# Kernel tuning notes

Measured on AMD Instinct MI355X. Metric: run time of the kernel, lower is better.

## Reference

```python
import jax, jax.numpy as jnp
import numpy as np

B, N, D, H = 8, 1024, 1024, 16
DH = D // H
SCALE = DH ** -0.5
NEG = -1e9


def setup_inputs() -> dict:
    key = jax.random.key(0)
    k1, k2, k3, k4 = jax.random.split(key, 4)
    x = jax.random.normal(k1, (B, N, D), dtype=jnp.float32)
    mask = jax.random.randint(k2, (B, N), 0, 2, dtype=jnp.int32)
    w_qkv = jax.random.normal(k3, (D, 3 * D), dtype=jnp.float32) * (D ** -0.5)
    w_out = jax.random.normal(k4, (D, D), dtype=jnp.float32) * (D ** -0.5)
    b_out = jnp.zeros((D,), dtype=jnp.float32)
    return {"x": x, "mask": mask, "w_qkv": w_qkv, "w_out": w_out, "b_out": b_out}


def reference(x, mask, w_qkv, w_out, b_out):
    b, n, d = x.shape
    qkv = x @ w_qkv  # [b, n, 3d]
    q, k, v = jnp.split(qkv, 3, axis=-1)
    # [b, n, d] -> [b, h, n, dh]
    reshape = lambda t: t.reshape(b, n, H, DH).transpose(0, 2, 1, 3)
    q, k, v = reshape(q), reshape(k), reshape(v)
    dots = jnp.einsum("bhqd,bhkd->bhqk", q, k) * SCALE  # [b, h, n, n]
    # mask [b, n] -> [b, 1, n]; broadcasts over heads and query dim (masks keys)
    m = (mask == 0)[:, None, None, :]
    dots = jnp.where(m, NEG, dots)
    attn = jax.nn.softmax(dots, axis=-1)
    out = jnp.einsum("bhqk,bhkd->bhqd", attn, v)  # [b, h, n, dh]
    out = out.transpose(0, 2, 1, 3).reshape(b, n, d)  # [b, n, d]
    out = out @ w_out + b_out
    return out, attn
```

## Files before the change

kernel.cpp:

```cpp
#include <hip/hip_runtime.h>
#include <hip/hip_bf16.h>

typedef unsigned short u16;
typedef __attribute__((ext_vector_type(8))) short bf16x8;
typedef __attribute__((ext_vector_type(4))) float f32x4;

#define DEVI __device__ __forceinline__

constexpr float SCALE = 0.125f;

DEVI float bf2f(u16 u) { unsigned v = ((unsigned)u) << 16; float f; __builtin_memcpy(&f, &v, 4); return f; }
DEVI u16 f2bf(float f) { __hip_bfloat16 h = __float2bfloat16(f); u16 u; __builtin_memcpy(&u, &h, 2); return u; }

DEVI void gload_lds16(const u16* g, u16* l) {
    __builtin_amdgcn_global_load_lds(
        (const __attribute__((address_space(1))) unsigned int*)g,
        (__attribute__((address_space(3))) unsigned int*)l, 16, 0, 0);
}

__global__ __launch_bounds__(256) void cast_f32_bf16(const float* __restrict__ in,
                                                     u16* __restrict__ out, int n) {
    int i = (blockIdx.x * 256 + threadIdx.x) * 4;
    if (i >= n) return;
    float4 v = *(const float4*)(in + i);
    ushort4 o;
    o.x = f2bf(v.x); o.y = f2bf(v.y); o.z = f2bf(v.z); o.w = f2bf(v.w);
    *(ushort4*)(out + i) = o;
}

__global__ __launch_bounds__(256) void transpose_f32_bf16(const float* __restrict__ in,
                                                          u16* __restrict__ out,
                                                          int R, int C) {
    __shared__ u16 t[64][65];
    int r0 = blockIdx.y * 64, c0 = blockIdx.x * 64;
    int tid = threadIdx.x;
    for (int i = 0; i < 16; i++) {
        int idx = tid + i * 256; int r = idx >> 6, c = idx & 63;
        t[r][c] = f2bf(in[(size_t)(r0 + r) * C + c0 + c]);
    }
    __syncthreads();
    for (int i = 0; i < 16; i++) {
        int idx = tid + i * 256; int c = idx >> 6, r = idx & 63;
        out[(size_t)(c0 + c) * R + r0 + r] = t[r][c];
    }
}

__global__ __launch_bounds__(256) void make_vt(const u16* __restrict__ qkv,
                                               u16* __restrict__ vt) {
    __shared__ u16 t[64][65];
    int bh = blockIdx.y; int b = bh >> 4, h = bh & 15;
    int n0 = blockIdx.x * 64;
    int tid = threadIdx.x;
    const u16* src = qkv + (size_t)b * 1024 * 3072 + 2048 + h * 64;
    for (int i = 0; i < 16; i++) {
        int idx = tid + i * 256; int n = idx >> 6, d = idx & 63;
        t[n][d] = src[(size_t)(n0 + n) * 3072 + d];
    }
    __syncthreads();
    u16* dst = vt + (size_t)bh * 64 * 1024;
    for (int i = 0; i < 16; i++) {
        int idx = tid + i * 256; int d = idx >> 6, n = idx & 63;
        dst[(size_t)d * 1024 + n0 + n] = t[n][d];
    }
}

template <bool BIAS, bool F32OUT>
__global__ __launch_bounds__(256) void gemm_bt(const u16* __restrict__ A,
                                               const u16* __restrict__ Bt,
                                               const float* __restrict__ bias,
                                               void* __restrict__ Cv,
                                               int M, int N, int K) {
    __shared__ alignas(16) u16 As[128 * 64];
    __shared__ alignas(16) u16 Bs[128 * 64];
    int tid = threadIdx.x;
    int wave = tid >> 6, lane = tid & 63, quad = lane >> 4, lm = lane & 15;
    int bm = blockIdx.y * 128, bn = blockIdx.x * 128;
    int wm = (wave >> 1) * 64, wn = (wave & 1) * 64;

    f32x4 acc[4][4];
    for (int i = 0; i < 4; i++) for (int j = 0; j < 4; j++) acc[i][j] = f32x4{0.f, 0.f, 0.f, 0.f};

    int lrow8 = lane >> 3;
    int lcol  = (lane & 7) * 8;

    for (int kb = 0; kb < K; kb += 64) {
        for (int i = 0; i < 4; i++) {
            int c = wave * 4 + i;
            int row = c * 8 + lrow8;
            gload_lds16(A  + (size_t)(bm + row) * K + kb + lcol, &As[c * 512 + lane * 8]);
            gload_lds16(Bt + (size_t)(bn + row) * K + kb + lcol, &Bs[c * 512 + lane * 8]);
        }
        __syncthreads();
        for (int ks = 0; ks < 2; ks++) {
            bf16x8 af[4], bfr[4];
            for (int mt = 0; mt < 4; mt++)
                af[mt] = *(const bf16x8*)(&As[(wm + mt * 16 + lm) * 64 + ks * 32 + quad * 8]);
            for (int nt = 0; nt < 4; nt++)
                bfr[nt] = *(const bf16x8*)(&Bs[(wn + nt * 16 + lm) * 64 + ks * 32 + quad * 8]);
            for (int mt = 0; mt < 4; mt++)
                for (int nt = 0; nt < 4; nt++)
                    acc[mt][nt] = __builtin_amdgcn_mfma_f32_16x16x32_bf16(
                        af[mt], bfr[nt], acc[mt][nt], 0, 0, 0);
        }
        __syncthreads();
    }
    for (int mt = 0; mt < 4; mt++)
        for (int nt = 0; nt < 4; nt++) {
            int col = bn + wn + nt * 16 + lm;
            float bv = BIAS ? bias[col] : 0.f;
            for (int r = 0; r < 4; r++) {
                int row = bm + wm + mt * 16 + quad * 4 + r;
                if (F32OUT) ((float*)Cv)[(size_t)row * N + col] = acc[mt][nt][r] + bv;
                else        ((u16*)Cv)[(size_t)row * N + col] = f2bf(acc[mt][nt][r] + bv);
            }
        }
}

__global__ __launch_bounds__(256) void attn_mfma(const u16* __restrict__ qkv,
                                                 const u16* __restrict__ vt,
                                                 const int* __restrict__ mask,
                                                 float* __restrict__ attn_out,
                                                 u16* __restrict__ o_ws) {
    __shared__ alignas(16) u16 Ks[2 * 64 * 64];
    __shared__ alignas(16) u16 Vs[2 * 64 * 64];
    constexpr int LDP = 72;
    __shared__ alignas(16) u16 Ps[64 * LDP];

    int tid = threadIdx.x;
    int wave = tid >> 6, lane = tid & 63, quad = lane >> 4, lm = lane & 15;

    int flat = blockIdx.y * gridDim.x + blockIdx.x;
    int swz = (flat & 7) * 256 + (flat >> 3);
    int bh = swz >> 4, qb = swz & 15;
    int b = bh >> 4, h = bh & 15;
    int qrow0 = qb * 64 + wave * 16;

    int srow = lane >> 3;
    int scol = (((lane & 7) ^ srow) << 3);

    const u16* kbase  = qkv + (size_t)b * 1024 * 3072 + 1024 + h * 64;
    const u16* vtbase = vt + (size_t)bh * 64 * 1024;
    const int* mrow   = mask + b * 1024;

    for (int i = 0; i < 2; i++) {
        int c = wave * 2 + i;
        gload_lds16(kbase + (size_t)(c * 8 + srow) * 3072 + scol, &Ks[c * 512 + lane * 8]);
    }

    bf16x8 qf[2];
    {
        const u16* qptr = qkv + (size_t)(b * 1024 + qrow0 + lm) * 3072 + h * 64 + quad * 8;
        qf[0] = *(const bf16x8*)(qptr);
        qf[1] = *(const bf16x8*)(qptr + 32);
    }

    int fsw0 = ((0 * 4 + quad) ^ (lm & 7)) << 3;
    int fsw1 = ((1 * 4 + quad) ^ (lm & 7)) << 3;

    float l_r[4] = {0.f, 0.f, 0.f, 0.f};
    int cur = 0;
    for (int kb = 0; kb < 16; kb++) {
        __syncthreads();
        if (kb < 15) {
            int nb = (cur ^ 1) * 4096;
            for (int i = 0; i < 2; i++) {
                int c = wave * 2 + i;
                gload_lds16(kbase + (size_t)((kb + 1) * 64 + c * 8 + srow) * 3072 + scol,
                            &Ks[nb + c * 512 + lane * 8]);
            }
        }
        const u16* K0 = &Ks[cur * 4096];
        f32x4 acc[4];
        for (int nt = 0; nt < 4; nt++) acc[nt] = f32x4{0.f, 0.f, 0.f, 0.f};
        for (int nt = 0; nt < 4; nt++) {
            bf16x8 kf0 = *(const bf16x8*)(&K0[(nt * 16 + lm) * 64 + fsw0]);
            bf16x8 kf1 = *(const bf16x8*)(&K0[(nt * 16 + lm) * 64 + fsw1]);
            acc[nt] = __builtin_amdgcn_mfma_f32_16x16x32_bf16(qf[0], kf0, acc[nt], 0, 0, 0);
            acc[nt] = __builtin_amdgcn_mfma_f32_16x16x32_bf16(qf[1], kf1, acc[nt], 0, 0, 0);
        }
        for (int nt = 0; nt < 4; nt++) {
            bool mk = (mrow[kb * 64 + nt * 16 + lm] != 0);
            for (int r = 0; r < 4; r++)
                l_r[r] += mk ? __expf(acc[nt][r] * SCALE) : 0.f;
        }
        cur ^= 1;
    }
    float invl[4];
    for (int r = 0; r < 4; r++) {
        float l = l_r[r];
        for (int s = 8; s >= 1; s >>= 1) l += __shfl_xor(l, s, 64);
        invl[r] = 1.0f / l;
    }

    for (int i = 0; i < 2; i++) {
        int c = wave * 2 + i;
        gload_lds16(kbase + (size_t)(c * 8 + srow) * 3072 + scol, &Ks[c * 512 + lane * 8]);
        gload_lds16(vtbase + (size_t)(c * 8 + srow) * 1024 + scol, &Vs[c * 512 + lane * 8]);
    }

    f32x4 oacc[4];
    for (int nt = 0; nt < 4; nt++) oacc[nt] = f32x4{0.f, 0.f, 0.f, 0.f};
    cur = 0;
    for (int kb = 0; kb < 16; kb++) {
        __syncthreads();
        if (kb < 15) {
            int nb = (cur ^ 1) * 4096;
            for (int i = 0; i < 2; i++) {
                int c = wave * 2 + i;
                gload_lds16(kbase + (size_t)((kb + 1) * 64 + c * 8 + srow) * 3072 + scol,
                            &Ks[nb + c * 512 + lane * 8]);
                gload_lds16(vtbase + (size_t)(c * 8 + srow) * 1024 + (kb + 1) * 64 + scol,
                            &Vs[nb + c * 512 + lane * 8]);
            }
        }
        const u16* K0 = &Ks[cur * 4096];
        const u16* V0 = &Vs[cur * 4096];
        f32x4 acc[4];
        for (int nt = 0; nt < 4; nt++) acc[nt] = f32x4{0.f, 0.f, 0.f, 0.f};
        for (int nt = 0; nt < 4; nt++) {
            bf16x8 kf0 = *(const bf16x8*)(&K0[(nt * 16 + lm) * 64 + fsw0]);
            bf16x8 kf1 = *(const bf16x8*)(&K0[(nt * 16 + lm) * 64 + fsw1]);
            acc[nt] = __builtin_amdgcn_mfma_f32_16x16x32_bf16(qf[0], kf0, acc[nt], 0, 0, 0);
            acc[nt] = __builtin_amdgcn_mfma_f32_16x16x32_bf16(qf[1], kf1, acc[nt], 0, 0, 0);
        }
        for (int nt = 0; nt < 4; nt++) {
            bool mk = (mrow[kb * 64 + nt * 16 + lm] != 0);
            for (int r = 0; r < 4; r++) {
                float p = mk ? __expf(acc[nt][r] * SCALE) * invl[r] : 0.f;
                attn_out[((size_t)bh * 1024 + qb * 64 + wave * 16 + quad * 4 + r) * 1024
                         + kb * 64 + nt * 16 + lm] = p;
                Ps[(wave * 16 + quad * 4 + r) * LDP + nt * 16 + lm] = f2bf(p);
            }
        }
        for (int ks = 0; ks < 2; ks++) {
            bf16x8 pf = *(const bf16x8*)(&Ps[(wave * 16 + lm) * LDP + ks * 32 + quad * 8]);
            int fsw = (ks == 0) ? fsw0 : fsw1;
            for (int nt = 0; nt < 4; nt++) {
                bf16x8 vf = *(const bf16x8*)(&V0[(nt * 16 + lm) * 64 + fsw]);
                oacc[nt] = __builtin_amdgcn_mfma_f32_16x16x32_bf16(pf, vf, oacc[nt], 0, 0, 0);
            }
        }
        cur ^= 1;
    }
    for (int nt = 0; nt < 4; nt++)
        for (int r = 0; r < 4; r++) {
            int row = qb * 64 + wave * 16 + quad * 4 + r;
            o_ws[(size_t)(b * 1024 + row) * 1024 + h * 64 + nt * 16 + lm] = f2bf(oacc[nt][r]);
        }
}

extern "C" void kernel_launch(void* const* d_in, const int* in_sizes, int n_in,
                              void* d_out, int out_size, void* d_ws, size_t ws_size,
                              hipStream_t stream) {
    const float* x    = (const float*)d_in[0];
    const int*   mask = (const int*)d_in[1];
    const float* wqkv = (const float*)d_in[2];
    const float* wout = (const float*)d_in[3];
    const float* bout = (const float*)d_in[4];

    float* out  = (float*)d_out;
    float* attn = out + (size_t)8192 * 1024;

    char* ws = (char*)d_ws;
    u16* xbf   = (u16*)(ws);
    u16* vt    = xbf;
    u16* qkv   = (u16*)(ws + 16777216);
    u16* o_ws  = (u16*)(ws + 67108864);
    u16* wqkvT = (u16*)(ws + 83886080);
    u16* woutT = (u16*)(ws + 90177536);

    cast_f32_bf16<<<dim3(8192), 256, 0, stream>>>(x, xbf, 8388608);
    transpose_f32_bf16<<<dim3(48, 16), 256, 0, stream>>>(wqkv, wqkvT, 1024, 3072);
    transpose_f32_bf16<<<dim3(16, 16), 256, 0, stream>>>(wout, woutT, 1024, 1024);
    gemm_bt<false, false><<<dim3(24, 64), 256, 0, stream>>>(xbf, wqkvT, nullptr, qkv, 8192, 3072, 1024);
    make_vt<<<dim3(16, 128), 256, 0, stream>>>(qkv, vt);
    attn_mfma<<<dim3(16, 128), 256, 0, stream>>>(qkv, vt, mask, attn, o_ws);
    gemm_bt<true, true><<<dim3(8, 64), 256, 0, stream>>>(o_ws, woutT, bout, out, 8192, 1024, 1024);
}
```

Before: 836.9 us.

## Split attention into row-sum and PV kernels, XOR-swizzle P tile

Splits the two-pass attention kernel into two launches. The first computes softmax row sums and writes inverse denominators to workspace, reusing the wqkvT region after the QKV GEMM has consumed it. The second recomputes the scores, writes attention probabilities and accumulates P·V. The lighter first kernel needs less LDS and fewer registers, which should raise occupancy, and the padded P tile is replaced with an XOR-swizzled unpadded layout to avoid LDS bank conflicts. The cost is an extra launch and a small workspace round trip.

```diff
diff --git a/kernel.cpp b/kernel.cpp
--- a/kernel.cpp
+++ b/kernel.cpp
@@ -116,15 +116,10 @@
         }
 }
 
-__global__ __launch_bounds__(256) void attn_mfma(const u16* __restrict__ qkv,
-                                                 const u16* __restrict__ vt,
+__global__ __launch_bounds__(256) void attn_lsum(const u16* __restrict__ qkv,
                                                  const int* __restrict__ mask,
-                                                 float* __restrict__ attn_out,
-                                                 u16* __restrict__ o_ws) {
+                                                 float* __restrict__ invl_ws) {
     __shared__ alignas(16) u16 Ks[2 * 64 * 64];
-    __shared__ alignas(16) u16 Vs[2 * 64 * 64];
-    constexpr int LDP = 72;
-    __shared__ alignas(16) u16 Ps[64 * LDP];
 
     int tid = threadIdx.x;
     int wave = tid >> 6, lane = tid & 63, quad = lane >> 4, lm = lane & 15;
@@ -138,9 +133,8 @@
     int srow = lane >> 3;
     int scol = (((lane & 7) ^ srow) << 3);
 
-    const u16* kbase  = qkv + (size_t)b * 1024 * 3072 + 1024 + h * 64;
-    const u16* vtbase = vt + (size_t)bh * 64 * 1024;
-    const int* mrow   = mask + b * 1024;
+    const u16* kbase = qkv + (size_t)b * 1024 * 3072 + 1024 + h * 64;
+    const int* mrow  = mask + b * 1024;
 
     for (int i = 0; i < 2; i++) {
         int c = wave * 2 + i;
@@ -153,7 +147,6 @@
         qf[0] = *(const bf16x8*)(qptr);
         qf[1] = *(const bf16x8*)(qptr + 32);
     }
-
     int fsw0 = ((0 * 4 + quad) ^ (lm & 7)) << 3;
     int fsw1 = ((1 * 4 + quad) ^ (lm & 7)) << 3;
 
@@ -185,12 +178,39 @@
         }
         cur ^= 1;
     }
-    float invl[4];
-    for (int r = 0; r < 4; r++) {
-        float l = l_r[r];
-        for (int s = 8; s >= 1; s >>= 1) l += __shfl_xor(l, s, 64);
-        invl[r] = 1.0f / l;
-    }
+    for (int r = 0; r < 4; r++)
+        for (int s = 8; s >= 1; s >>= 1) l_r[r] += __shfl_xor(l_r[r], s, 64);
+    if (lm == 0) {
+        float4 v; v.x = 1.f / l_r[0]; v.y = 1.f / l_r[1]; v.z = 1.f / l_r[2]; v.w = 1.f / l_r[3];
+        *(float4*)(invl_ws + (size_t)bh * 1024 + qb * 64 + wave * 16 + quad * 4) = v;
+    }
+}
+
+__global__ __launch_bounds__(256) void attn_pv(const u16* __restrict__ qkv,
+                                               const u16* __restrict__ vt,
+                                               const int* __restrict__ mask,
+                                               const float* __restrict__ invl_ws,
+                                               float* __restrict__ attn_out,
+                                               u16* __restrict__ o_ws) {
+    __shared__ alignas(16) u16 Ks[2 * 64 * 64];
+    __shared__ alignas(16) u16 Vs[2 * 64 * 64];
+    __shared__ alignas(16) u16 Ps[64 * 64];
+
+    int tid = threadIdx.x;
+    int wave = tid >> 6, lane = tid & 63, quad = lane >> 4, lm = lane & 15;
+
+    int flat = blockIdx.y * gridDim.x + blockIdx.x;
+    int swz = (flat & 7) * 256 + (flat >> 3);
+    int bh = swz >> 4, qb = swz & 15;
+    int b = bh >> 4, h = bh & 15;
+    int qrow0 = qb * 64 + wave * 16;
+
+    int srow = lane >> 3;
+    int scol = (((lane & 7) ^ srow) << 3);
+
+    const u16* kbase  = qkv + (size_t)b * 1024 * 3072 + 1024 + h * 64;
+    const u16* vtbase = vt + (size_t)bh * 64 * 1024;
+    const int* mrow   = mask + b * 1024;
 
     for (int i = 0; i < 2; i++) {
         int c = wave * 2 + i;
@@ -198,9 +218,23 @@
         gload_lds16(vtbase + (size_t)(c * 8 + srow) * 1024 + scol, &Vs[c * 512 + lane * 8]);
     }
 
+    bf16x8 qf[2];
+    {
+        const u16* qptr = qkv + (size_t)(b * 1024 + qrow0 + lm) * 3072 + h * 64 + quad * 8;
+        qf[0] = *(const bf16x8*)(qptr);
+        qf[1] = *(const bf16x8*)(qptr + 32);
+    }
+    float invl[4];
+    for (int r = 0; r < 4; r++)
+        invl[r] = invl_ws[(size_t)bh * 1024 + qrow0 + quad * 4 + r];
+
+    int fsw0 = ((0 * 4 + quad) ^ (lm & 7)) << 3;
+    int fsw1 = ((1 * 4 + quad) ^ (lm & 7)) << 3;
+    int psw  = (lm & 7) << 3;
+
     f32x4 oacc[4];
     for (int nt = 0; nt < 4; nt++) oacc[nt] = f32x4{0.f, 0.f, 0.f, 0.f};
-    cur = 0;
+    int cur = 0;
     for (int kb = 0; kb < 16; kb++) {
         __syncthreads();
         if (kb < 15) {
@@ -229,11 +263,14 @@
                 float p = mk ? __expf(acc[nt][r] * SCALE) * invl[r] : 0.f;
                 attn_out[((size_t)bh * 1024 + qb * 64 + wave * 16 + quad * 4 + r) * 1024
                          + kb * 64 + nt * 16 + lm] = p;
-                Ps[(wave * 16 + quad * 4 + r) * LDP + nt * 16 + lm] = f2bf(p);
+                int pr = wave * 16 + quad * 4 + r;
+                int pidx = (pr * 64 + nt * 16 + lm) ^ (((quad * 4 + r) & 7) << 3);
+                Ps[pidx] = f2bf(p);
             }
         }
         for (int ks = 0; ks < 2; ks++) {
-            bf16x8 pf = *(const bf16x8*)(&Ps[(wave * 16 + lm) * LDP + ks * 32 + quad * 8]);
+            int ridx = ((wave * 16 + lm) * 64 + ks * 32 + quad * 8) ^ psw;
+            bf16x8 pf = *(const bf16x8*)(&Ps[ridx]);
             int fsw = (ks == 0) ? fsw0 : fsw1;
             for (int nt = 0; nt < 4; nt++) {
                 bf16x8 vf = *(const bf16x8*)(&V0[(nt * 16 + lm) * 64 + fsw]);
@@ -267,6 +304,7 @@
     u16* qkv   = (u16*)(ws + 16777216);
     u16* o_ws  = (u16*)(ws + 67108864);
     u16* wqkvT = (u16*)(ws + 83886080);
+    float* invl = (float*)(ws + 83886080);
     u16* woutT = (u16*)(ws + 90177536);
 
     cast_f32_bf16<<<dim3(8192), 256, 0, stream>>>(x, xbf, 8388608);
@@ -274,6 +312,7 @@
     transpose_f32_bf16<<<dim3(16, 16), 256, 0, stream>>>(wout, woutT, 1024, 1024);
     gemm_bt<false, false><<<dim3(24, 64), 256, 0, stream>>>(xbf, wqkvT, nullptr, qkv, 8192, 3072, 1024);
     make_vt<<<dim3(16, 128), 256, 0, stream>>>(qkv, vt);
-    attn_mfma<<<dim3(16, 128), 256, 0, stream>>>(qkv, vt, mask, attn, o_ws);
+    attn_lsum<<<dim3(16, 128), 256, 0, stream>>>(qkv, mask, invl);
+    attn_pv<<<dim3(16, 128), 256, 0, stream>>>(qkv, vt, mask, invl, attn, o_ws);
     gemm_bt<true, true><<<dim3(8, 64), 256, 0, stream>>>(o_ws, woutT, bout, out, 8192, 1024, 1024);
 }
```

Result: no change. 822.7 us (-1.7%).
